# Kernel tuning notes

Hardware: AMD Instinct MI355X
Metric: run time of the kernel (lower is better)

Reference implementation:

```python
import jax, jax.numpy as jnp
import numpy as np
import math
from jax import lax

DIM = 128
D_STATE = 16
D_CONV = 4
EXPAND = 2
NSLICES = 16
D_INNER = EXPAND * DIM          # 256
DT_RANK = math.ceil(DIM / 16)   # 8
B_, H_, W_ = 4, 64, 64
L = H_ * W_                     # 4096


def silu(x):
    return x * jax.nn.sigmoid(x)


def causal_conv1d(x, w, b):
    # x: (b, d, l), w: (d, k) depthwise, b: (d,)  -- causal, output length l
    l = x.shape[-1]
    xp = jnp.pad(x, ((0, 0), (0, 0), (D_CONV - 1, 0)))
    y = sum(w[None, :, k, None] * xp[:, :, k:k + l] for k in range(D_CONV))
    return y + b[None, :, None]


def selective_scan(u, delta, A, B, C):
    # u, delta: (b, d, l); A: (d, n); B, C: (b, n, l)
    bsz, d, l = u.shape
    n = A.shape[1]
    u_t = u.transpose(2, 0, 1)      # (l, b, d)
    d_t = delta.transpose(2, 0, 1)  # (l, b, d)
    B_t = B.transpose(2, 0, 1)      # (l, b, n)
    C_t = C.transpose(2, 0, 1)      # (l, b, n)

    def step(h, inp):
        u_, de_, b_, c_ = inp
        dA = jnp.exp(de_[..., None] * A)                    # (b, d, n)
        h = h * dA + (de_ * u_)[..., None] * b_[:, None, :]  # (b, d, n)
        y = jnp.einsum('bdn,bn->bd', h, c_)
        return h, y

    h0 = jnp.zeros((bsz, d, n), u.dtype)
    _, ys = lax.scan(step, h0, (u_t, d_t, B_t, C_t))
    return ys.transpose(1, 2, 0)  # (b, d, l)


def mamba_dir(xz, conv_w, conv_b, x_proj_w, dt_w, dt_b, A_log, Dp):
    # one directional Mamba branch (conv + S6 scan + silu(z) gating), returns (b, d_inner, l)
    x, z = jnp.split(xz, 2, axis=1)
    x = silu(causal_conv1d(x, conv_w, conv_b))
    x_dbl = jnp.einsum('rd,bdl->brl', x_proj_w, x)          # (b, dt_rank+2n, l)
    dt_raw = x_dbl[:, :DT_RANK]
    Bm = x_dbl[:, DT_RANK:DT_RANK + D_STATE]
    Cm = x_dbl[:, DT_RANK + D_STATE:]
    delta = jax.nn.softplus(jnp.einsum('dr,brl->bdl', dt_w, dt_raw) + dt_b[None, :, None])
    A = -jnp.exp(A_log)
    y = selective_scan(x, delta, A, Bm, Cm)
    y = y + Dp[None, :, None] * x
    return y * silu(z)


def setup_inputs() -> dict:
    key = jax.random.key(0)
    ks = iter(jax.random.split(key, 40))

    def rn(shape, scale=0.02):
        return jax.random.normal(next(ks), shape, dtype=jnp.float32) * scale

    inp = {"x_in": jax.random.normal(next(ks), (B_, H_, W_, DIM), dtype=jnp.float32)}
    inp["in_proj_w"] = rn((2 * D_INNER, DIM))
    for suf in ["", "_b", "_s"]:
        inp["conv_w" + suf] = rn((D_INNER, D_CONV), 0.1)
        inp["conv_b" + suf] = rn((D_INNER,), 0.1)
        inp["x_proj_w" + suf] = rn((DT_RANK + 2 * D_STATE, D_INNER))
        inp["dt_proj_w" + suf] = rn((D_INNER, DT_RANK), 0.1)
        inp["dt_proj_b" + suf] = rn((D_INNER,), 0.1)
        inp["A_log" + suf] = jnp.log(jnp.tile(jnp.arange(1, D_STATE + 1, dtype=jnp.float32), (D_INNER, 1)))
        inp["D" + suf] = jnp.ones((D_INNER,), jnp.float32)
    inp["out_proj_w"] = rn((DIM, D_INNER))
    return inp


def reference(x_in, in_proj_w, conv_w, conv_b, x_proj_w, dt_proj_w, dt_proj_b, A_log, D,
              conv_w_b, conv_b_b, x_proj_w_b, dt_proj_w_b, dt_proj_b_b, A_log_b, D_b,
              conv_w_s, conv_b_s, x_proj_w_s, dt_proj_w_s, dt_proj_b_s, A_log_s, D_s,
              out_proj_w):
    b, h, w, c = x_in.shape
    l = h * w
    x = x_in.reshape(b, l, c)
    xz = jnp.einsum('pd,bld->bpl', in_proj_w, x)  # (b, 2*d_inner, l)

    # forward scan
    y_f = mamba_dir(xz, conv_w, conv_b, x_proj_w, dt_proj_w, dt_proj_b, A_log, D)
    # backward scan (flip along length)
    y_b = jnp.flip(mamba_dir(jnp.flip(xz, -1), conv_w_b, conv_b_b, x_proj_w_b,
                             dt_proj_w_b, dt_proj_b_b, A_log_b, D_b), -1)
    # interleaved-slice scan: chunk length into NSLICES pieces, stack, flatten
    m = l // NSLICES
    xz_s = xz.reshape(b, 2 * D_INNER, NSLICES, m).swapaxes(-1, -2).reshape(b, 2 * D_INNER, l)
    y_s = mamba_dir(xz_s, conv_w_s, conv_b_s, x_proj_w_s, dt_proj_w_s, dt_proj_b_s, A_log_s, D_s)
    y_s = y_s.reshape(b, D_INNER, m, NSLICES).swapaxes(-1, -2).reshape(b, D_INNER, l)

    y = y_f + y_b + y_s
    out = jnp.einsum('od,bdl->blo', out_proj_w, y)
    return out.reshape(b, h, w, c)
```

## Files before the change

### kernel.cpp

```cpp
#include <hip/hip_runtime.h>
#include <math.h>

#define LSEQ 4096

#define XZ_OFF   0ULL
#define XZ_SZ    (4ULL * 4096 * 512)
#define U_OFF    (XZ_OFF + XZ_SZ)
#define DIR_SZ   (4ULL * 256 * 4096)
#define DELTA_OFF (U_OFF + 3ULL * DIR_SZ)
#define BC_OFF   (DELTA_OFF + 3ULL * DIR_SZ)
#define BC_SZ    (4ULL * 4096 * 32)
#define WTIN_OFF DELTA_OFF
#define WTOUT_OFF U_OFF

typedef float v2f __attribute__((ext_vector_type(2)));
typedef float v4f __attribute__((ext_vector_type(4)));

__device__ __forceinline__ float sigmoidf_(float x) { return 1.0f / (1.0f + __expf(-x)); }
__device__ __forceinline__ float siluf_(float x)    { return x * sigmoidf_(x); }

__device__ __forceinline__ float fast_exp2_asm(float x) {
    float r;
    asm volatile("v_exp_f32 %0, %1\n\ts_nop 0" : "=v"(r) : "v"(x));
    return r;
}
#if defined(__has_builtin)
#if __has_builtin(__builtin_amdgcn_exp2f)
#define EXP2(x) __builtin_amdgcn_exp2f(x)
#else
#define EXP2(x) fast_exp2_asm(x)
#endif
#else
#define EXP2(x) fast_exp2_asm(x)
#endif

__device__ __forceinline__ float softplus_fast(float x) {
    float t = EXP2(1.44269504f * x);
    float r = 0.69314718f * __log2f(1.0f + t);
    return (x > 20.0f) ? x : r;
}

__device__ __forceinline__ int perm_idx(int dir, int j) {
    if (dir == 0) return j;
    if (dir == 1) return 4095 - j;
    return ((j & 15) << 8) | (j >> 4);
}

#define DPP_MOV(x, ctrl) __int_as_float(__builtin_amdgcn_update_dpp(0, __float_as_int(x), (ctrl), 0xF, 0xF, true))

__global__ __launch_bounds__(256) void transpose_in_kernel(const float* __restrict__ w,
                                                           float* __restrict__ wT) {
    int idx = blockIdx.x * 256 + threadIdx.x;
    int p = idx >> 7, c = idx & 127;
    wT[(size_t)c * 512 + p] = w[(size_t)p * 128 + c];
}

__global__ __launch_bounds__(256) void inproj_kernel(const float* __restrict__ x,
                              const float* __restrict__ wT,
                              float* __restrict__ xz) {
    const int b = blockIdx.y;
    const int l0 = blockIdx.x * 16;
    __shared__ float xs[128 * 20];
    for (int idx = threadIdx.x; idx < 16 * 128; idx += 256) {
        int li = idx >> 7, c = idx & 127;
        xs[c * 20 + li] = x[((size_t)(b * 4096 + l0 + li)) * 128 + c];
    }
    __syncthreads();
    const int p0 = (threadIdx.x & 127) * 4;
    const int g8 = (threadIdx.x >> 7) * 8;
    float acc[4][8];
    #pragma unroll
    for (int j = 0; j < 4; ++j)
        #pragma unroll
        for (int k = 0; k < 8; ++k) acc[j][k] = 0.0f;
    for (int c = 0; c < 128; ++c) {
        float4 wv = *(const float4*)(wT + (size_t)c * 512 + p0);
        const float* xp = xs + c * 20 + g8;
        float4 x0 = *(const float4*)(xp);
        float4 x1 = *(const float4*)(xp + 4);
        float xv[8] = {x0.x, x0.y, x0.z, x0.w, x1.x, x1.y, x1.z, x1.w};
        float wj[4] = {wv.x, wv.y, wv.z, wv.w};
        #pragma unroll
        for (int j = 0; j < 4; ++j)
            #pragma unroll
            for (int k = 0; k < 8; ++k) acc[j][k] += wj[j] * xv[k];
    }
    #pragma unroll
    for (int k = 0; k < 8; ++k) {
        float4 s; s.x = acc[0][k]; s.y = acc[1][k]; s.z = acc[2][k]; s.w = acc[3][k];
        *(float4*)(xz + ((size_t)(b * 4096 + l0 + g8 + k)) * 512 + p0) = s;
    }
}

__global__ __launch_bounds__(256, 4) void front_kernel(float* __restrict__ ws,
        const float* __restrict__ xw0, const float* __restrict__ xw1, const float* __restrict__ xw2,
        const float* __restrict__ dw0, const float* __restrict__ dw1, const float* __restrict__ dw2,
        const float* __restrict__ db0, const float* __restrict__ db1, const float* __restrict__ db2,
        const float* __restrict__ cw0, const float* __restrict__ cb0,
        const float* __restrict__ cw1, const float* __restrict__ cb1,
        const float* __restrict__ cw2, const float* __restrict__ cb2) {
    const int l0 = blockIdx.x * 32, b = blockIdx.y, dir = blockIdx.z;
    const float* xw = (dir == 0) ? xw0 : (dir == 1) ? xw1 : xw2;
    const float* dw = (dir == 0) ? dw0 : (dir == 1) ? dw1 : dw2;
    const float* db = (dir == 0) ? db0 : (dir == 1) ? db1 : db2;
    const float* cw = (dir == 0) ? cw0 : (dir == 1) ? cw1 : cw2;
    const float* cb = (dir == 0) ? cb0 : (dir == 1) ? cb1 : cb2;
    const float* xzb = ws + XZ_OFF + (size_t)b * 4096 * 512;
    float* ub      = ws + U_OFF + (size_t)dir * DIR_SZ + (size_t)b * 256 * 4096;
    float* deltab  = ws + DELTA_OFF + (size_t)dir * DIR_SZ + (size_t)b * 256 * 4096;
    float* Bf      = ws + BC_OFF + (size_t)dir * BC_SZ;
    float* Cf      = Bf + BC_SZ / 2;

    __shared__ float xt[32 * 256];
    __shared__ float xws[40 * 36];
    float* ut = xt;
    float* xd = xt;

    for (int idx = threadIdx.x; idx < 32 * 64; idx += 256) {
        int k = idx >> 6, dq = idx & 63;
        int j = l0 + k;
        int row = (dir == 0) ? j : (dir == 1) ? (4095 - j) : (((j & 15) << 8) | (j >> 4));
        float4 v = *(const float4*)(xzb + (size_t)row * 512 + dq * 4);
        *(float4*)(xt + k * 256 + dq * 4) = v;
    }

    const int d = threadIdx.x;
    float h0 = 0.0f, h1 = 0.0f, h2 = 0.0f;
    {
        int j = l0 - 3;
        if (j >= 0) h0 = xzb[(size_t)perm_idx(dir, j) * 512 + d];
        j = l0 - 2;
        if (j >= 0) h1 = xzb[(size_t)perm_idx(dir, j) * 512 + d];
        j = l0 - 1;
        if (j >= 0) h2 = xzb[(size_t)perm_idx(dir, j) * 512 + d];
    }
    __syncthreads();

    const float w0 = cw[d * 4 + 0], w1 = cw[d * 4 + 1], w2 = cw[d * 4 + 2], w3 = cw[d * 4 + 3];
    const float bb = cb[d];
    float r[32];
    #pragma unroll
    for (int li = 0; li < 32; ++li) {
        float cur = xt[li * 256 + d];
        r[li] = siluf_(bb + w0 * h0 + w1 * h1 + w2 * h2 + w3 * cur);
        h0 = h1; h1 = h2; h2 = cur;
    }
    {
        float* urow = ub + (size_t)d * 4096 + l0;
        #pragma unroll
        for (int q = 0; q < 8; ++q) {
            float4 v; v.x = r[q*4]; v.y = r[q*4+1]; v.z = r[q*4+2]; v.w = r[q*4+3];
            *(float4*)(urow + q * 4) = v;
        }
    }
    __syncthreads();

    #pragma unroll
    for (int li = 0; li < 32; ++li)
        ut[li * 256 + 4 * (((d >> 2) ^ (li & 7))) + (d & 3)] = r[li];

    {
        const int rg = threadIdx.x >> 5;
        const int li = threadIdx.x & 31;
        float acc[5];
        #pragma unroll
        for (int j = 0; j < 5; ++j) acc[j] = 0.0f;
        const int sw = (li & 7);
        for (int ct = 0; ct < 8; ++ct) {
            __syncthreads();
            for (int idx = threadIdx.x; idx < 320; idx += 256) {
                int rr = idx >> 3, q = (idx & 7) * 4;
                *(float4*)(xws + rr * 36 + q) = *(const float4*)(xw + (size_t)rr * 256 + ct * 32 + q);
            }
            __syncthreads();
            #pragma unroll
            for (int t = 0; t < 8; ++t) {
                const int qq = t ^ sw;
                float4 uv = *(const float4*)(ut + li * 256 + ct * 32 + 4 * qq);
                #pragma unroll
                for (int j = 0; j < 5; ++j) {
                    float4 wv = *(const float4*)(xws + (rg * 5 + j) * 36 + 4 * t);
                    acc[j] += wv.x * uv.x + wv.y * uv.y + wv.z * uv.z + wv.w * uv.w;
                }
            }
        }
        __syncthreads();
        #pragma unroll
        for (int j = 0; j < 5; ++j) xd[(rg * 5 + j) * 33 + li] = acc[j];
    }
    __syncthreads();

    {
        const int wv = threadIdx.x >> 6;
        const int lane = threadIdx.x & 63;
        const int n = lane >> 2, lq = lane & 3;
        #pragma unroll
        for (int j = 0; j < 2; ++j) {
            int l4 = (l0 >> 2) + j * 4 + wv;
            int li = (j * 4 + wv) * 4 + lq;
            size_t base = (((size_t)b * 1024 + l4) * 16 + n) * 4 + lq;
            Bf[base] = xd[(8 + n) * 33 + li];
            Cf[base] = xd[(24 + n) * 33 + li];
        }
    }
    {
        const int li = threadIdx.x & 31;
        float xr8[8];
        #pragma unroll
        for (int rr = 0; rr < 8; ++rr) xr8[rr] = xd[rr * 33 + li];
        #pragma unroll
        for (int k = 0; k < 32; ++k) {
            int dd = ((threadIdx.x + k * 256) >> 5);
            float4 wa = *(const float4*)(dw + dd * 8);
            float4 wb = *(const float4*)(dw + dd * 8 + 4);
            float acc = db[dd]
                + wa.x * xr8[0] + wa.y * xr8[1] + wa.z * xr8[2] + wa.w * xr8[3]
                + wb.x * xr8[4] + wb.y * xr8[5] + wb.z * xr8[6] + wb.w * xr8[7];
            deltab[(size_t)dd * 4096 + l0 + li] = softplus_fast(acc);
        }
    }
}

__global__ __launch_bounds__(1024, 8) void scan_kernel(float* __restrict__ ws,
                            const float* __restrict__ Al0, const float* __restrict__ Dp0,
                            const float* __restrict__ Al1, const float* __restrict__ Dp1,
                            const float* __restrict__ Al2, const float* __restrict__ Dp2) {
    const int d0 = blockIdx.x * 2, b = blockIdx.y, dir = blockIdx.z;
    const float* Al = (dir == 0) ? Al0 : (dir == 1) ? Al1 : Al2;
    const float* Dp = (dir == 0) ? Dp0 : (dir == 1) ? Dp1 : Dp2;
    const int n  = threadIdx.x & 15;
    const int d2 = (threadIdx.x >> 4) & 1;
    const int c  = threadIdx.x >> 5;
    const int nl = n & 7;
    const int d = d0 + d2;
    const float Ane = -1.44269504f * __expf(Al[d * 16 + n]);
    const v2f AneD = {Ane, Ane};
    const float Dd = Dp[d];
    const float* ubase = ws + U_OFF + (size_t)dir * DIR_SZ + ((size_t)(b * 256 + d0)) * 4096;
    float* dbase = ws + DELTA_OFF + (size_t)dir * DIR_SZ + ((size_t)(b * 256 + d0)) * 4096;
    float* drow = dbase + (size_t)d2 * 4096;

    __shared__ float sdu[2][32 * 260 + 8];
    __shared__ float ps[2][1032];

    for (int i = threadIdx.x; i < 2048; i += 1024) {
        int dsl = i >> 10, ii = i & 1023;
        float4 dv = ((const float4*)(dbase + (size_t)dsl * 4096))[ii];
        float4 uv = ((const float4*)(ubase + (size_t)dsl * 4096))[ii];
        int l = ii * 4;
        float* p = sdu[dsl] + (l >> 7) * 260 + (l & 127) * 2;
        *(float4*)(p) = dv; *(float4*)(p + 4) = uv;
    }
    __syncthreads();

    const v4f* Bq = (const v4f*)(ws + BC_OFF + (size_t)dir * BC_SZ)
                       + ((size_t)b * 1024 + c * 32) * 16 + n;
    const v4f* Cq = (const v4f*)(ws + BC_OFF + (size_t)dir * BC_SZ + BC_SZ / 2)
                       + ((size_t)b * 1024 + c * 32) * 16 + n;
    const v4f* sp = (const v4f*)(sdu[d2] + c * 260);
    float* Psh = ps[d2];
    float* Ssh = ps[d2] + 512;

    float S = 0.0f;
    v2f ds2 = {0.0f, 0.0f};
    #pragma unroll 8
    for (int k4 = 0; k4 < 32; ++k4) {
        v4f dq = sp[k4 * 2], uq = sp[k4 * 2 + 1];
        v4f Bv = Bq[(size_t)k4 * 16];
        v2f du0 = dq.xy * uq.xy;
        v2f du1 = dq.zw * uq.zw;
        v2f t0 = AneD * dq.xy;
        v2f t1 = AneD * dq.zw;
        v2f p0 = du0 * Bv.xy;
        v2f p1 = du1 * Bv.zw;
        ds2 += dq.xy + dq.zw;
        S = __builtin_fmaf(S, EXP2(t0.x), p0.x);
        S = __builtin_fmaf(S, EXP2(t0.y), p0.y);
        S = __builtin_fmaf(S, EXP2(t1.x), p1.x);
        S = __builtin_fmaf(S, EXP2(t1.y), p1.y);
    }
    Ssh[c * 16 + n] = S;
    Psh[c * 16 + n] = EXP2(Ane * (ds2.x + ds2.y));
    __syncthreads();
    float h = 0.0f;
    #pragma unroll 2
    for (int k = 0; k < c; ++k) h = __builtin_fmaf(h, Psh[k * 16 + n], Ssh[k * 16 + n]);

    for (int g = 0; g < 16; ++g) {
        const int j0 = g * 8 + nl;
        float uo = sdu[d2][c * 260 + ((j0 >> 2) << 3) + 4 + (j0 & 3)];
        v4f dq0 = sp[g * 4 + 0], uq0 = sp[g * 4 + 1];
        v4f dq1 = sp[g * 4 + 2], uq1 = sp[g * 4 + 3];
        v4f Bv0 = Bq[(size_t)(g * 2) * 16], Bv1 = Bq[(size_t)(g * 2 + 1) * 16];
        v4f Cv0 = Cq[(size_t)(g * 2) * 16], Cv1 = Cq[(size_t)(g * 2 + 1) * 16];
        v2f t0 = AneD * dq0.xy, t1 = AneD * dq0.zw;
        v2f t2 = AneD * dq1.xy, t3 = AneD * dq1.zw;
        v2f q0 = dq0.xy * uq0.xy, q1 = dq0.zw * uq0.zw;
        v2f q2 = dq1.xy * uq1.xy, q3 = dq1.zw * uq1.zw;
        v2f p0 = q0 * Bv0.xy, p1 = q1 * Bv0.zw;
        v2f p2 = q2 * Bv1.xy, p3 = q3 * Bv1.zw;
        float e0 = EXP2(t0.x), e1 = EXP2(t0.y);
        float e2 = EXP2(t1.x), e3 = EXP2(t1.y);
        float e4 = EXP2(t2.x), e5 = EXP2(t2.y);
        float e6 = EXP2(t3.x), e7 = EXP2(t3.y);
        float ya0, ya1, ya2, ya3, ya4, ya5, ya6, ya7;
        h = __builtin_fmaf(h, e0, p0.x); ya0 = h * Cv0.x;
        h = __builtin_fmaf(h, e1, p0.y); ya1 = h * Cv0.y;
        h = __builtin_fmaf(h, e2, p1.x); ya2 = h * Cv0.z;
        h = __builtin_fmaf(h, e3, p1.y); ya3 = h * Cv0.w;
        h = __builtin_fmaf(h, e4, p2.x); ya4 = h * Cv1.x;
        h = __builtin_fmaf(h, e5, p2.y); ya5 = h * Cv1.y;
        h = __builtin_fmaf(h, e6, p3.x); ya6 = h * Cv1.z;
        h = __builtin_fmaf(h, e7, p3.y); ya7 = h * Cv1.w;
        ya0 += DPP_MOV(ya0, 0xB1); ya1 += DPP_MOV(ya1, 0xB1);
        ya2 += DPP_MOV(ya2, 0xB1); ya3 += DPP_MOV(ya3, 0xB1);
        ya4 += DPP_MOV(ya4, 0xB1); ya5 += DPP_MOV(ya5, 0xB1);
        ya6 += DPP_MOV(ya6, 0xB1); ya7 += DPP_MOV(ya7, 0xB1);
        float z0 = (n & 1) ? ya1 : ya0;
        float z1 = (n & 1) ? ya3 : ya2;
        float z2 = (n & 1) ? ya5 : ya4;
        float z3 = (n & 1) ? ya7 : ya6;
        z0 += DPP_MOV(z0, 0x4E); z1 += DPP_MOV(z1, 0x4E);
        z2 += DPP_MOV(z2, 0x4E); z3 += DPP_MOV(z3, 0x4E);
        float w0 = (n & 2) ? z1 : z0;
        float w1 = (n & 2) ? z3 : z2;
        w0 += DPP_MOV(w0, 0x124); w1 += DPP_MOV(w1, 0x124);
        w0 += DPP_MOV(w0, 0x128); w1 += DPP_MOV(w1, 0x128);
        float ysel = (n & 4) ? w1 : w0;
        if (n < 8) drow[perm_idx(dir, c * 128 + j0)] = ysel + Dd * uo;
    }
}

__global__ __launch_bounds__(256) void transpose_w_kernel(const float* __restrict__ ow,
                                                          float* __restrict__ wT) {
    int idx = blockIdx.x * 256 + threadIdx.x;
    int o = idx >> 8, d = idx & 255;
    wT[(size_t)d * 128 + o] = ow[(size_t)o * 256 + d];
}

__global__ __launch_bounds__(256) void epilogue_kernel(const float* __restrict__ ws,
                                const float* __restrict__ wT,
                                float* __restrict__ out) {
    const int l0 = blockIdx.x * 16, b = blockIdx.y;
    __shared__ float yt[256 * 20];
    __shared__ float wts[64 * 128];
    const float* yf = ws + DELTA_OFF;
    const float* yb = ws + DELTA_OFF + DIR_SZ;
    const float* ysd = ws + DELTA_OFF + 2 * DIR_SZ;
    const float* xzb = ws + XZ_OFF + (size_t)b * 4096 * 512;

    for (int idx = threadIdx.x; idx < 256 * 4; idx += 256) {
        int d = idx >> 2, q = (idx & 3) * 4;
        size_t ro = ((size_t)(b * 256 + d)) * 4096 + l0 + q;
        float4 vf = *(const float4*)(yf + ro);
        float4 vb = *(const float4*)(yb + ro);
        float4 vs = *(const float4*)(ysd + ro);
        float4 s; s.x = vf.x + vb.x + vs.x; s.y = vf.y + vb.y + vs.y;
        s.z = vf.z + vb.z + vs.z; s.w = vf.w + vb.w + vs.w;
        *(float4*)(yt + d * 20 + q) = s;
    }
    __syncthreads();
    {
        const int d = threadIdx.x;
        #pragma unroll 4
        for (int li = 0; li < 16; ++li) {
            float z = xzb[(size_t)(l0 + li) * 512 + 256 + d];
            yt[d * 20 + li] *= siluf_(z);
        }
    }

    const int o0 = (threadIdx.x & 31) * 4;
    const int lp = (threadIdx.x >> 5) * 2;
    float a0[4], a1[4];
    #pragma unroll
    for (int j = 0; j < 4; ++j) { a0[j] = 0.0f; a1[j] = 0.0f; }
    for (int dt = 0; dt < 4; ++dt) {
        __syncthreads();
        for (int idx = threadIdx.x; idx < 64 * 32; idx += 256) {
            int dd = idx >> 5, q = (idx & 31) * 4;
            *(float4*)(wts + dd * 128 + q) = *(const float4*)(wT + (size_t)(dt * 64 + dd) * 128 + q);
        }
        __syncthreads();
        #pragma unroll 4
        for (int dl = 0; dl < 64; ++dl) {
            float4 w = *(const float4*)(wts + dl * 128 + o0);
            float2 y = *(const float2*)(yt + (dt * 64 + dl) * 20 + lp);
            a0[0] += w.x * y.x; a0[1] += w.y * y.x; a0[2] += w.z * y.x; a0[3] += w.w * y.x;
            a1[0] += w.x * y.y; a1[1] += w.y * y.y; a1[2] += w.z * y.y; a1[3] += w.w * y.y;
        }
    }
    float4 s0; s0.x = a0[0]; s0.y = a0[1]; s0.z = a0[2]; s0.w = a0[3];
    float4 s1; s1.x = a1[0]; s1.y = a1[1]; s1.z = a1[2]; s1.w = a1[3];
    *(float4*)(out + ((size_t)(b * 4096 + l0 + lp)) * 128 + o0) = s0;
    *(float4*)(out + ((size_t)(b * 4096 + l0 + lp + 1)) * 128 + o0) = s1;
}

extern "C" void kernel_launch(void* const* d_in, const int* in_sizes, int n_in,
                              void* d_out, int out_size, void* d_ws, size_t ws_size,
                              hipStream_t stream) {
    const float* x_in = (const float*)d_in[0];
    const float* ipw  = (const float*)d_in[1];
    const float* cw[3]  = {(const float*)d_in[2],  (const float*)d_in[9],  (const float*)d_in[16]};
    const float* cb[3]  = {(const float*)d_in[3],  (const float*)d_in[10], (const float*)d_in[17]};
    const float* xpw[3] = {(const float*)d_in[4],  (const float*)d_in[11], (const float*)d_in[18]};
    const float* dtw[3] = {(const float*)d_in[5],  (const float*)d_in[12], (const float*)d_in[19]};
    const float* dtb[3] = {(const float*)d_in[6],  (const float*)d_in[13], (const float*)d_in[20]};
    const float* alog[3]= {(const float*)d_in[7],  (const float*)d_in[14], (const float*)d_in[21]};
    const float* dp[3]  = {(const float*)d_in[8],  (const float*)d_in[15], (const float*)d_in[22]};
    const float* ow   = (const float*)d_in[23];
    float* ws  = (float*)d_ws;
    float* out = (float*)d_out;

    transpose_in_kernel<<<dim3(256), 256, 0, stream>>>(ipw, ws + WTIN_OFF);
    inproj_kernel<<<dim3(256, 4), 256, 0, stream>>>(x_in, ws + WTIN_OFF, ws);
    front_kernel<<<dim3(128, 4, 3), 256, 0, stream>>>(ws,
        xpw[0], xpw[1], xpw[2], dtw[0], dtw[1], dtw[2], dtb[0], dtb[1], dtb[2],
        cw[0], cb[0], cw[1], cb[1], cw[2], cb[2]);
    scan_kernel<<<dim3(128, 4, 3), 1024, 0, stream>>>(ws,
        alog[0], dp[0], alog[1], dp[1], alog[2], dp[2]);
    transpose_w_kernel<<<dim3(128), 256, 0, stream>>>(ow, ws + WTOUT_OFF);
    epilogue_kernel<<<dim3(256, 4), 256, 0, stream>>>(ws, ws + WTOUT_OFF, out);
}
```

Measured before the change: 348.8 us.

## Halve front kernel block size, fuse out-proj transpose, recoalesce scan loads

The front kernel now runs with 128 threads per block, so each thread handles two channels for the conv and two sequence positions for the x_proj GEMV, which raises per-thread work and register use. The separate transpose_w kernel is dropped and the epilogue transposes out_proj weights into padded shared memory, removing one launch and a global round trip. The scan kernel's shared-memory staging of delta/u is reordered so consecutive threads read contiguous float4s. The trade-off is fewer threads per block in the front kernel and scattered shared-memory stores in the epilogue.

```diff
diff --git a/kernel.cpp b/kernel.cpp
--- a/kernel.cpp
+++ b/kernel.cpp
@@ -11,7 +11,6 @@
 #define BC_OFF   (DELTA_OFF + 3ULL * DIR_SZ)
 #define BC_SZ    (4ULL * 4096 * 32)
 #define WTIN_OFF DELTA_OFF
-#define WTOUT_OFF U_OFF
 
 typedef float v2f __attribute__((ext_vector_type(2)));
 typedef float v4f __attribute__((ext_vector_type(4)));
@@ -92,7 +91,7 @@
     }
 }
 
-__global__ __launch_bounds__(256, 4) void front_kernel(float* __restrict__ ws,
+__global__ __launch_bounds__(128, 2) void front_kernel(float* __restrict__ ws,
         const float* __restrict__ xw0, const float* __restrict__ xw1, const float* __restrict__ xw2,
         const float* __restrict__ dw0, const float* __restrict__ dw1, const float* __restrict__ dw2,
         const float* __restrict__ db0, const float* __restrict__ db1, const float* __restrict__ db2,
@@ -116,7 +115,7 @@
     float* ut = xt;
     float* xd = xt;
 
-    for (int idx = threadIdx.x; idx < 32 * 64; idx += 256) {
+    for (int idx = threadIdx.x; idx < 32 * 64; idx += 128) {
         int k = idx >> 6, dq = idx & 63;
         int j = l0 + k;
         int row = (dir == 0) ? j : (dir == 1) ? (4095 - j) : (((j & 15) << 8) | (j >> 4));
@@ -124,51 +123,64 @@
         *(float4*)(xt + k * 256 + dq * 4) = v;
     }
 
-    const int d = threadIdx.x;
-    float h0 = 0.0f, h1 = 0.0f, h2 = 0.0f;
+    const int dA = threadIdx.x;
+    const int dB = threadIdx.x + 128;
+    float h0a = 0.f, h1a = 0.f, h2a = 0.f, h0b = 0.f, h1b = 0.f, h2b = 0.f;
     {
         int j = l0 - 3;
-        if (j >= 0) h0 = xzb[(size_t)perm_idx(dir, j) * 512 + d];
+        if (j >= 0) { int rr = perm_idx(dir, j);
+            h0a = xzb[(size_t)rr * 512 + dA]; h0b = xzb[(size_t)rr * 512 + dB]; }
         j = l0 - 2;
-        if (j >= 0) h1 = xzb[(size_t)perm_idx(dir, j) * 512 + d];
+        if (j >= 0) { int rr = perm_idx(dir, j);
+            h1a = xzb[(size_t)rr * 512 + dA]; h1b = xzb[(size_t)rr * 512 + dB]; }
         j = l0 - 1;
-        if (j >= 0) h2 = xzb[(size_t)perm_idx(dir, j) * 512 + d];
-    }
-    __syncthreads();
-
-    const float w0 = cw[d * 4 + 0], w1 = cw[d * 4 + 1], w2 = cw[d * 4 + 2], w3 = cw[d * 4 + 3];
-    const float bb = cb[d];
-    float r[32];
+        if (j >= 0) { int rr = perm_idx(dir, j);
+            h2a = xzb[(size_t)rr * 512 + dA]; h2b = xzb[(size_t)rr * 512 + dB]; }
+    }
+    __syncthreads();
+
+    const float w0a = cw[dA * 4 + 0], w1a = cw[dA * 4 + 1], w2a = cw[dA * 4 + 2], w3a = cw[dA * 4 + 3];
+    const float w0b = cw[dB * 4 + 0], w1b = cw[dB * 4 + 1], w2b = cw[dB * 4 + 2], w3b = cw[dB * 4 + 3];
+    const float bba = cb[dA], bbb = cb[dB];
+    float ra[32], rb[32];
     #pragma unroll
     for (int li = 0; li < 32; ++li) {
-        float cur = xt[li * 256 + d];
-        r[li] = siluf_(bb + w0 * h0 + w1 * h1 + w2 * h2 + w3 * cur);
-        h0 = h1; h1 = h2; h2 = cur;
-    }
-    {
-        float* urow = ub + (size_t)d * 4096 + l0;
+        float ca = xt[li * 256 + dA];
+        float cbv = xt[li * 256 + dB];
+        ra[li] = siluf_(bba + w0a * h0a + w1a * h1a + w2a * h2a + w3a * ca);
+        rb[li] = siluf_(bbb + w0b * h0b + w1b * h1b + w2b * h2b + w3b * cbv);
+        h0a = h1a; h1a = h2a; h2a = ca;
+        h0b = h1b; h1b = h2b; h2b = cbv;
+    }
+    {
+        float* urowA = ub + (size_t)dA * 4096 + l0;
+        float* urowB = ub + (size_t)dB * 4096 + l0;
         #pragma unroll
         for (int q = 0; q < 8; ++q) {
-            float4 v; v.x = r[q*4]; v.y = r[q*4+1]; v.z = r[q*4+2]; v.w = r[q*4+3];
-            *(float4*)(urow + q * 4) = v;
+            float4 va; va.x = ra[q*4]; va.y = ra[q*4+1]; va.z = ra[q*4+2]; va.w = ra[q*4+3];
+            *(float4*)(urowA + q * 4) = va;
+            float4 vb; vb.x = rb[q*4]; vb.y = rb[q*4+1]; vb.z = rb[q*4+2]; vb.w = rb[q*4+3];
+            *(float4*)(urowB + q * 4) = vb;
         }
     }
     __syncthreads();
 
     #pragma unroll
-    for (int li = 0; li < 32; ++li)
-        ut[li * 256 + 4 * (((d >> 2) ^ (li & 7))) + (d & 3)] = r[li];
-
-    {
-        const int rg = threadIdx.x >> 5;
-        const int li = threadIdx.x & 31;
-        float acc[5];
-        #pragma unroll
-        for (int j = 0; j < 5; ++j) acc[j] = 0.0f;
-        const int sw = (li & 7);
+    for (int li = 0; li < 32; ++li) {
+        ut[li * 256 + 4 * (((dA >> 2) ^ (li & 7))) + (dA & 3)] = ra[li];
+        ut[li * 256 + 4 * (((dB >> 2) ^ (li & 7))) + (dB & 3)] = rb[li];
+    }
+
+    {
+        const int rg = threadIdx.x >> 4;
+        const int lp = threadIdx.x & 15;
+        float acc[5][2];
+        #pragma unroll
+        for (int j = 0; j < 5; ++j) { acc[j][0] = 0.0f; acc[j][1] = 0.0f; }
+        const int sw = lp & 7;
         for (int ct = 0; ct < 8; ++ct) {
             __syncthreads();
-            for (int idx = threadIdx.x; idx < 320; idx += 256) {
+            for (int idx = threadIdx.x; idx < 320; idx += 128) {
                 int rr = idx >> 3, q = (idx & 7) * 4;
                 *(float4*)(xws + rr * 36 + q) = *(const float4*)(xw + (size_t)rr * 256 + ct * 32 + q);
             }
@@ -176,28 +188,33 @@
             #pragma unroll
             for (int t = 0; t < 8; ++t) {
                 const int qq = t ^ sw;
-                float4 uv = *(const float4*)(ut + li * 256 + ct * 32 + 4 * qq);
+                float4 u0 = *(const float4*)(ut + lp * 256 + ct * 32 + 4 * qq);
+                float4 u1 = *(const float4*)(ut + (lp + 16) * 256 + ct * 32 + 4 * qq);
                 #pragma unroll
                 for (int j = 0; j < 5; ++j) {
                     float4 wv = *(const float4*)(xws + (rg * 5 + j) * 36 + 4 * t);
-                    acc[j] += wv.x * uv.x + wv.y * uv.y + wv.z * uv.z + wv.w * uv.w;
+                    acc[j][0] += wv.x * u0.x + wv.y * u0.y + wv.z * u0.z + wv.w * u0.w;
+                    acc[j][1] += wv.x * u1.x + wv.y * u1.y + wv.z * u1.z + wv.w * u1.w;
                 }
             }
         }
         __syncthreads();
         #pragma unroll
-        for (int j = 0; j < 5; ++j) xd[(rg * 5 + j) * 33 + li] = acc[j];
-    }
-    __syncthreads();
-
-    {
-        const int wv = threadIdx.x >> 6;
+        for (int j = 0; j < 5; ++j) {
+            xd[(rg * 5 + j) * 33 + lp] = acc[j][0];
+            xd[(rg * 5 + j) * 33 + lp + 16] = acc[j][1];
+        }
+    }
+    __syncthreads();
+
+    {
+        const int wv2 = threadIdx.x >> 6;
         const int lane = threadIdx.x & 63;
         const int n = lane >> 2, lq = lane & 3;
         #pragma unroll
-        for (int j = 0; j < 2; ++j) {
-            int l4 = (l0 >> 2) + j * 4 + wv;
-            int li = (j * 4 + wv) * 4 + lq;
+        for (int j = 0; j < 4; ++j) {
+            int l4 = (l0 >> 2) + j * 2 + wv2;
+            int li = (j * 2 + wv2) * 4 + lq;
             size_t base = (((size_t)b * 1024 + l4) * 16 + n) * 4 + lq;
             Bf[base] = xd[(8 + n) * 33 + li];
             Cf[base] = xd[(24 + n) * 33 + li];
@@ -205,12 +222,13 @@
     }
     {
         const int li = threadIdx.x & 31;
+        const int rgp = threadIdx.x >> 5;
         float xr8[8];
         #pragma unroll
         for (int rr = 0; rr < 8; ++rr) xr8[rr] = xd[rr * 33 + li];
-        #pragma unroll
-        for (int k = 0; k < 32; ++k) {
-            int dd = ((threadIdx.x + k * 256) >> 5);
+        #pragma unroll 8
+        for (int k = 0; k < 64; ++k) {
+            int dd = k * 4 + rgp;
             float4 wa = *(const float4*)(dw + dd * 8);
             float4 wb = *(const float4*)(dw + dd * 8 + 4);
             float acc = db[dd]
@@ -234,7 +252,7 @@
     const int nl = n & 7;
     const int d = d0 + d2;
     const float Ane = -1.44269504f * __expf(Al[d * 16 + n]);
-    const v2f AneD = {Ane, Ane};
+    v2f AneD; AneD.x = Ane; AneD.y = Ane;
     const float Dd = Dp[d];
     const float* ubase = ws + U_OFF + (size_t)dir * DIR_SZ + ((size_t)(b * 256 + d0)) * 4096;
     float* dbase = ws + DELTA_OFF + (size_t)dir * DIR_SZ + ((size_t)(b * 256 + d0)) * 4096;
@@ -243,13 +261,16 @@
     __shared__ float sdu[2][32 * 260 + 8];
     __shared__ float ps[2][1032];
 
-    for (int i = threadIdx.x; i < 2048; i += 1024) {
-        int dsl = i >> 10, ii = i & 1023;
-        float4 dv = ((const float4*)(dbase + (size_t)dsl * 4096))[ii];
-        float4 uv = ((const float4*)(ubase + (size_t)dsl * 4096))[ii];
-        int l = ii * 4;
-        float* p = sdu[dsl] + (l >> 7) * 260 + (l & 127) * 2;
-        *(float4*)(p) = dv; *(float4*)(p + 4) = uv;
+    for (int gid = threadIdx.x; gid < 4096; gid += 1024) {
+        int dsl = gid >> 11;
+        int rem = gid & 2047;
+        int row = rem >> 6;
+        int s = rem & 63;
+        int fq = row * 32 + (s >> 1);
+        const float* srcb = (s & 1) ? (const float*)(ubase + (size_t)dsl * 4096)
+                                    : (const float*)(dbase + (size_t)dsl * 4096);
+        float4 v = ((const float4*)srcb)[fq];
+        *(float4*)(sdu[dsl] + row * 260 + s * 4) = v;
     }
     __syncthreads();
 
@@ -262,7 +283,7 @@
     float* Ssh = ps[d2] + 512;
 
     float S = 0.0f;
-    v2f ds2 = {0.0f, 0.0f};
+    v2f ds2; ds2.x = 0.0f; ds2.y = 0.0f;
     #pragma unroll 8
     for (int k4 = 0; k4 < 32; ++k4) {
         v4f dq = sp[k4 * 2], uq = sp[k4 * 2 + 1];
@@ -331,19 +352,12 @@
     }
 }
 
-__global__ __launch_bounds__(256) void transpose_w_kernel(const float* __restrict__ ow,
-                                                          float* __restrict__ wT) {
-    int idx = blockIdx.x * 256 + threadIdx.x;
-    int o = idx >> 8, d = idx & 255;
-    wT[(size_t)d * 128 + o] = ow[(size_t)o * 256 + d];
-}
-
 __global__ __launch_bounds__(256) void epilogue_kernel(const float* __restrict__ ws,
-                                const float* __restrict__ wT,
+                                const float* __restrict__ ow,
                                 float* __restrict__ out) {
     const int l0 = blockIdx.x * 16, b = blockIdx.y;
     __shared__ float yt[256 * 20];
-    __shared__ float wts[64 * 128];
+    __shared__ float wts[64 * 129];
     const float* yf = ws + DELTA_OFF;
     const float* yb = ws + DELTA_OFF + DIR_SZ;
     const float* ysd = ws + DELTA_OFF + 2 * DIR_SZ;
@@ -376,14 +390,19 @@
     for (int j = 0; j < 4; ++j) { a0[j] = 0.0f; a1[j] = 0.0f; }
     for (int dt = 0; dt < 4; ++dt) {
         __syncthreads();
-        for (int idx = threadIdx.x; idx < 64 * 32; idx += 256) {
-            int dd = idx >> 5, q = (idx & 31) * 4;
-            *(float4*)(wts + dd * 128 + q) = *(const float4*)(wT + (size_t)(dt * 64 + dd) * 128 + q);
+        for (int idx = threadIdx.x; idx < 2048; idx += 256) {
+            int o = idx >> 4;
+            int dq = (idx & 15) * 4;
+            float4 v = *(const float4*)(ow + (size_t)o * 256 + dt * 64 + dq);
+            wts[(dq + 0) * 129 + o] = v.x;
+            wts[(dq + 1) * 129 + o] = v.y;
+            wts[(dq + 2) * 129 + o] = v.z;
+            wts[(dq + 3) * 129 + o] = v.w;
         }
         __syncthreads();
         #pragma unroll 4
         for (int dl = 0; dl < 64; ++dl) {
-            float4 w = *(const float4*)(wts + dl * 128 + o0);
+            float4 w = *(const float4*)(wts + dl * 129 + o0);
             float2 y = *(const float2*)(yt + (dt * 64 + dl) * 20 + lp);
             a0[0] += w.x * y.x; a0[1] += w.y * y.x; a0[2] += w.z * y.x; a0[3] += w.w * y.x;
             a1[0] += w.x * y.y; a1[1] += w.y * y.y; a1[2] += w.z * y.y; a1[3] += w.w * y.y;
@@ -413,11 +432,10 @@
 
     transpose_in_kernel<<<dim3(256), 256, 0, stream>>>(ipw, ws + WTIN_OFF);
     inproj_kernel<<<dim3(256, 4), 256, 0, stream>>>(x_in, ws + WTIN_OFF, ws);
-    front_kernel<<<dim3(128, 4, 3), 256, 0, stream>>>(ws,
+    front_kernel<<<dim3(128, 4, 3), 128, 0, stream>>>(ws,
         xpw[0], xpw[1], xpw[2], dtw[0], dtw[1], dtw[2], dtb[0], dtb[1], dtb[2],
         cw[0], cb[0], cw[1], cb[1], cw[2], cb[2]);
     scan_kernel<<<dim3(128, 4, 3), 1024, 0, stream>>>(ws,
         alog[0], dp[0], alog[1], dp[1], alog[2], dp[2]);
-    transpose_w_kernel<<<dim3(128), 256, 0, stream>>>(ow, ws + WTOUT_OFF);
-    epilogue_kernel<<<dim3(256, 4), 256, 0, stream>>>(ws, ws + WTOUT_OFF, out);
-}
+    epilogue_kernel<<<dim3(256, 4), 256, 0, stream>>>(ws, ow, out);
+}
```

Result: slower. 389.7 us (+11.7%).
